# Kernel optimization log

Hardware: AMD Instinct MI355X
Metric: run time of the kernel (lower is better)

The kernel has to match this reference:

```python
import jax, jax.numpy as jnp
import numpy as np

B, N, D, C, H = 32, 36, 2048, 4, 512  # batch, regions, feat dim, coord dim, fusion hidden


def setup_inputs() -> dict:
    key = jax.random.key(0)
    ks = jax.random.split(key, 8)
    w = lambda k, sh: jax.random.normal(k, sh, dtype=jnp.float32) * 0.02
    return {
        "mm": jax.random.normal(ks[0], (B, N, D), dtype=jnp.float32),
        "coords": jax.random.uniform(ks[1], (B, N, C), dtype=jnp.float32),
        # MLB fusion params for coords: z = (x@W_cl * y@W_cr) @ W_cout
        "W_cl": w(ks[2], (C, H)),
        "W_cr": w(ks[3], (C, H)),
        "W_cout": w(ks[4], (H, D)),
        # MLB fusion params for features
        "W_fl": w(ks[5], (D, H)),
        "W_fr": w(ks[6], (D, H)),
        "W_fout": w(ks[7], (H, D)),
    }


def reference(mm, coords, W_cl, W_cr, W_cout, W_fl, W_fr, W_fout):
    # Project once per region (avoids projecting inside the N*N expand).
    cl = coords @ W_cl            # [B,N,H]
    cr = coords @ W_cr            # [B,N,H]
    fl = mm @ W_fl                # [B,N,H]
    fr = mm @ W_fr                # [B,N,H]
    # All-pairs bilinear fusion: Rij = f_coord(c_i, c_j) + f_feat(m_i, m_j)
    pair_c = cl[:, :, None, :] * cr[:, None, :, :]   # [B,N,N,H]
    pair_f = fl[:, :, None, :] * fr[:, None, :, :]   # [B,N,N,H]
    Rij = (jnp.einsum('bijh,hd->bijd', pair_c, W_cout)
           + jnp.einsum('bijh,hd->bijd', pair_f, W_fout))  # [B,N,N,D]
    # agg['type'] == 'max': reduce over the right (j) region axis
    mm_new = Rij.max(axis=2)      # [B,N,D]
    # residual
    return mm_new + mm
```

## Files before the change

### kernel.cpp

```cpp
#include <hip/hip_runtime.h>


typedef __attribute__((ext_vector_type(8))) short short8;
typedef __attribute__((ext_vector_type(4))) short short4v;
typedef __attribute__((ext_vector_type(4))) float f32x4;

__device__ __forceinline__ float bf2f(unsigned short h) {
  return __uint_as_float(((unsigned int)h) << 16);
}
__device__ __forceinline__ unsigned short f2bf(float f) {
  unsigned int u = __float_as_uint(f);
  u += 0x7FFFu + ((u >> 16) & 1u);
  return (unsigned short)(u >> 16);
}
__device__ __forceinline__ void gl2lds16(const void* g, void* l) {
  __builtin_amdgcn_global_load_lds(
      (const __attribute__((address_space(1))) unsigned int*)g,
      (__attribute__((address_space(3))) unsigned int*)l, 16, 0, 0);
}

__global__ __launch_bounds__(256) void k_prep(
    const float* __restrict__ mm, const float* __restrict__ Wfout,
    const float* __restrict__ Wcl, const float* __restrict__ Wcr,
    const float* __restrict__ Wcout, const float* __restrict__ Wfl,
    const float* __restrict__ Wfr, unsigned short* __restrict__ mmb,
    unsigned short* __restrict__ WS, unsigned short* __restrict__ WS2) {
  const int bid = blockIdx.x;
  if (bid < 2304) {
    int idx = bid * 256 + threadIdx.x;
    int row = idx >> 9, h = idx & 511;
    float4 m4 = *(const float4*)(mm + (size_t)row * 2048 + h * 4);
    short4v o;
    o[0] = (short)f2bf(m4.x); o[1] = (short)f2bf(m4.y);
    o[2] = (short)f2bf(m4.z); o[3] = (short)f2bf(m4.w);
    *(short4v*)(mmb + (size_t)row * 2048 + h * 4) = o;
  } else {
    int gi = (bid - 2304) * 256 + threadIdx.x;
    if (gi < 139264) {
      int n = gi & 15, qv = (gi >> 4) & 3, rest = gi >> 6;
      int kc = rest % 17, g2 = rest / 17;
      int d = g2 * 16 + n;
      short8 o;
      if (kc < 16) {
        int kbase = kc * 32 + qv * 8;
        const float* src = Wfout + (size_t)kbase * 2048 + d;
#pragma unroll
        for (int e = 0; e < 8; ++e) o[e] = (short)f2bf(src[(size_t)e * 2048]);
      } else if (qv < 2) {
        float acc[8];
#pragma unroll
        for (int e = 0; e < 8; ++e) acc[e] = 0.f;
        for (int h = 0; h < 512; ++h) {
          float wo = Wcout[(size_t)h * 2048 + d];
          float c0 = Wcl[(qv * 2 + 0) * 512 + h] * wo;
          float c1 = Wcl[(qv * 2 + 1) * 512 + h] * wo;
          float r0 = Wcr[h], r1 = Wcr[512 + h];
          float r2 = Wcr[1024 + h], r3 = Wcr[1536 + h];
          acc[0] += c0 * r0; acc[1] += c0 * r1;
          acc[2] += c0 * r2; acc[3] += c0 * r3;
          acc[4] += c1 * r0; acc[5] += c1 * r1;
          acc[6] += c1 * r2; acc[7] += c1 * r3;
        }
#pragma unroll
        for (int e = 0; e < 8; ++e) o[e] = (short)f2bf(acc[e]);
      } else {
#pragma unroll
        for (int e = 0; e < 8; ++e) o[e] = 0;
      }
      *(short8*)(WS + (size_t)gi * 8) = o;
    } else {
      int gj = gi - 139264;
      int n = gj & 15, qv = (gj >> 4) & 3, kc = (gj >> 6) & 63, cg = gj >> 12;
      int col = cg * 16 + n;
      int dbase = kc * 32 + qv * 8;
      const float* src = (col < 512) ? (Wfl + (size_t)dbase * 512 + col)
                                     : (Wfr + (size_t)dbase * 512 + (col - 512));
      short8 o;
#pragma unroll
      for (int e = 0; e < 8; ++e) o[e] = (short)f2bf(src[(size_t)e * 512]);
      *(short8*)(WS2 + (size_t)gj * 8) = o;
    }
  }
}

__global__ __launch_bounds__(256) void k_proj_feat(
    const unsigned short* __restrict__ mmb, const unsigned short* __restrict__ WS2,
    unsigned short* __restrict__ Fl, unsigned short* __restrict__ Fr) {
  const int tid = threadIdx.x;
  const int lane = tid & 63, w = tid >> 6;
  const int n = lane & 15, q = lane >> 4;
  const int m0 = blockIdx.y * 16;
  const int cg = blockIdx.x * 4 + w;
  const int c0 = cg * 16;

  f32x4 acc = {0.f, 0.f, 0.f, 0.f};
#pragma unroll 4
  for (int kc = 0; kc < 64; ++kc) {
    short8 a = *(const short8*)(mmb + (size_t)(m0 + n) * 2048 + kc * 32 + q * 8);
    short8 b = *(const short8*)(WS2 + (size_t)(cg * 64 + kc) * 512 + lane * 8);
    acc = __builtin_amdgcn_mfma_f32_16x16x32_bf16(a, b, acc, 0, 0, 0);
  }
#pragma unroll
  for (int e = 0; e < 4; ++e) {
    int row = m0 + q * 4 + e;
    int col = c0 + n;
    unsigned short v = f2bf(acc[e]);
    if (col < 512) Fl[(size_t)row * 512 + col] = v;
    else           Fr[(size_t)row * 512 + (col - 512)] = v;
  }
}

__global__ __launch_bounds__(256) void k_prod(
    const unsigned short* __restrict__ Fl, const unsigned short* __restrict__ Fr,
    const float* __restrict__ coords, unsigned short* __restrict__ Pf) {
  int idx = blockIdx.x * 256 + threadIdx.x;
  int lane = idx & 63;
  int gran = idx >> 6;
  int qg = gran / 153;
  int rem = gran - qg * 153;
  int kc = rem / 9;
  int t = rem - kc * 9;
  int n = lane & 15, q = lane >> 4;
  int b = qg / 9;
  int g, j;
  if (t < 8) { g = qg * 4 + (t >> 1); j = (t & 1) * 16 + n; }
  else       { g = qg * 4 + (n >> 2); j = 32 + (n & 3); }
  int rowj = b * 36 + j;
  short8 p;
  if (kc < 16) {
    int k0 = kc * 32 + q * 8;
    short8 cl8 = *(const short8*)(Fl + (size_t)g * 512 + k0);
    short8 cr8 = *(const short8*)(Fr + (size_t)rowj * 512 + k0);
#pragma unroll
    for (int e = 0; e < 8; ++e)
      p[e] = (short)f2bf(bf2f((unsigned short)cl8[e]) * bf2f((unsigned short)cr8[e]));
  } else if (q < 2) {
    float4 ci = *(const float4*)(coords + (size_t)g * 4);
    float4 cj = *(const float4*)(coords + (size_t)rowj * 4);
#pragma unroll
    for (int e = 0; e < 8; ++e) {
      int a = q * 2 + (e >> 2);
      float ca = (a == 0) ? ci.x : (a == 1) ? ci.y : (a == 2) ? ci.z : ci.w;
      float cb = ((e & 3) == 0) ? cj.x : ((e & 3) == 1) ? cj.y
               : ((e & 3) == 2) ? cj.z : cj.w;
      p[e] = (short)f2bf(ca * cb);
    }
  } else {
#pragma unroll
    for (int e = 0; e < 8; ++e) p[e] = 0;
  }
  *(short8*)(Pf + (size_t)idx * 8) = p;
}

__global__ __launch_bounds__(512, 4) void k_pairwise(
    const unsigned short* __restrict__ Pf, const unsigned short* __restrict__ WS,
    const float* __restrict__ mm, float* __restrict__ out) {
  __shared__ __align__(16) unsigned short lB[2][9 * 512];

  const int tid = threadIdx.x;
  const int lane = tid & 63, w = tid >> 6;
  const int n = lane & 15, q = lane >> 4;
  const int bx = blockIdx.x;
  const int x = bx & 7;
  const int m = bx >> 3;
  const int dt = m & 7;
  const int qg = x * 36 + (m >> 3);
  const int g0 = qg * 4;

  f32x4 acc[9][2];
#pragma unroll
  for (int t = 0; t < 9; ++t)
#pragma unroll
    for (int r = 0; r < 2; ++r) acc[t][r] = (f32x4){0.f, 0.f, 0.f, 0.f};

  const unsigned short* Abase = WS + ((size_t)(dt * 16 + w * 2) * 17) * 512 + lane * 8;
  const unsigned short* Bbase = Pf + (size_t)qg * 17 * 9 * 512;

  gl2lds16(Bbase + (size_t)w * 512 + lane * 8, &lB[0][w * 512]);
  if (w == 0) gl2lds16(Bbase + (size_t)8 * 512 + lane * 8, &lB[0][8 * 512]);
  __syncthreads();

#pragma unroll 2
  for (int kc = 0; kc < 16; ++kc) {
    const int buf = kc & 1;
    const unsigned short* bn = Bbase + (size_t)((kc + 1) * 9) * 512 + lane * 8;
    gl2lds16(bn + (size_t)w * 512, &lB[buf ^ 1][w * 512]);
    if (w == 0) gl2lds16(bn + (size_t)8 * 512, &lB[buf ^ 1][8 * 512]);

    short8 a0 = *(const short8*)(Abase + (size_t)kc * 512);
    short8 a1 = *(const short8*)(Abase + (size_t)(17 + kc) * 512);

    short8 bb[9];
#pragma unroll
    for (int t = 0; t < 9; ++t)
      bb[t] = *(const short8*)(&lB[buf][t * 512 + lane * 8]);
#pragma unroll
    for (int t = 0; t < 9; ++t) {
      acc[t][0] = __builtin_amdgcn_mfma_f32_16x16x32_bf16(a0, bb[t], acc[t][0], 0, 0, 0);
      acc[t][1] = __builtin_amdgcn_mfma_f32_16x16x32_bf16(a1, bb[t], acc[t][1], 0, 0, 0);
    }
    __syncthreads();
  }

  {
    short8 a0 = *(const short8*)(Abase + (size_t)16 * 512);
    short8 a1 = *(const short8*)(Abase + (size_t)(17 + 16) * 512);
    short8 bb[9];
#pragma unroll
    for (int t = 0; t < 9; ++t)
      bb[t] = *(const short8*)(&lB[0][t * 512 + lane * 8]);
#pragma unroll
    for (int t = 0; t < 9; ++t) {
      acc[t][0] = __builtin_amdgcn_mfma_f32_16x16x32_bf16(a0, bb[t], acc[t][0], 0, 0, 0);
      acc[t][1] = __builtin_amdgcn_mfma_f32_16x16x32_bf16(a1, bb[t], acc[t][1], 0, 0, 0);
    }
  }

#pragma unroll
  for (int r = 0; r < 2; ++r) {
#pragma unroll
    for (int e = 0; e < 4; ++e) {
      float vs = acc[8][r][e];
#pragma unroll
      for (int ii = 0; ii < 4; ++ii) {
        float v = fmaxf(acc[ii * 2][r][e], acc[ii * 2 + 1][r][e]);
        v = fmaxf(v, ((n >> 2) == ii) ? vs : -1e30f);
#pragma unroll
        for (int s = 1; s < 16; s <<= 1) v = fmaxf(v, __shfl_xor(v, s, 64));
        if (n == 0) {
          int d = dt * 256 + w * 32 + r * 16 + q * 4 + e;
          size_t o = (size_t)(g0 + ii) * 2048 + d;
          out[o] = v + mm[o];
        }
      }
    }
  }
}

extern "C" void kernel_launch(void* const* d_in, const int* in_sizes, int n_in,
                              void* d_out, int out_size, void* d_ws, size_t ws_size,
                              hipStream_t stream) {
  const float* mm     = (const float*)d_in[0];
  const float* coords = (const float*)d_in[1];
  const float* Wcl    = (const float*)d_in[2];
  const float* Wcr    = (const float*)d_in[3];
  const float* Wcout  = (const float*)d_in[4];
  const float* Wfl    = (const float*)d_in[5];
  const float* Wfr    = (const float*)d_in[6];
  const float* Wfout  = (const float*)d_in[7];
  float* out = (float*)d_out;

  unsigned short* Fl  = (unsigned short*)d_ws;
  unsigned short* Fr  = Fl + (size_t)1152 * 512;
  unsigned short* WS  = Fr + (size_t)1152 * 512;
  unsigned short* WS2 = WS + (size_t)139264 * 8;
  unsigned short* mmb = WS2 + (size_t)262144 * 8;
  unsigned short* Pf  = mmb + (size_t)1152 * 2048;

  k_prep<<<2304 + 1568, 256, 0, stream>>>(mm, Wfout, Wcl, Wcr, Wcout,
                                          Wfl, Wfr, mmb, WS, WS2);
  k_proj_feat<<<dim3(16, 72), 256, 0, stream>>>(mmb, WS2, Fl, Fr);
  k_prod<<<11016, 256, 0, stream>>>(Fl, Fr, coords, Pf);
  k_pairwise<<<2304, 512, 0, stream>>>(Pf, WS, mm, out);
}
```

Before: 355.0 us.

## Triple-buffer B tiles, preload ninth tile group, prefetch A fragments one step ahead

Replaces the double-buffered LDS staging with a three-slot ring for the first eight B tiles, so loads run two k-steps ahead. The ninth tile column for all k-steps is loaded into LDS once up front. The A fragments are register-prefetched one step ahead, and the full __syncthreads is swapped for an explicit vmcnt wait plus s_barrier. The goal is to hide global-to-LDS latency and remove stalls at the barrier, at the cost of more LDS per block, which may reduce occupancy.

New measurement: 303.8 us. 14.4% less time.

```diff
diff --git a/kernel.cpp b/kernel.cpp
--- a/kernel.cpp
+++ b/kernel.cpp
@@ -155,7 +155,8 @@
 __global__ __launch_bounds__(512, 4) void k_pairwise(
     const unsigned short* __restrict__ Pf, const unsigned short* __restrict__ WS,
     const float* __restrict__ mm, float* __restrict__ out) {
-  __shared__ __align__(16) unsigned short lB[2][9 * 512];
+  __shared__ __align__(16) unsigned short ring[3][8 * 512];
+  __shared__ __align__(16) unsigned short g8[17 * 512];
 
   const int tid = threadIdx.x;
   const int lane = tid & 63, w = tid >> 6;
@@ -176,45 +177,60 @@
   const unsigned short* Abase = WS + ((size_t)(dt * 16 + w * 2) * 17) * 512 + lane * 8;
   const unsigned short* Bbase = Pf + (size_t)qg * 17 * 9 * 512;
 
-  gl2lds16(Bbase + (size_t)w * 512 + lane * 8, &lB[0][w * 512]);
-  if (w == 0) gl2lds16(Bbase + (size_t)8 * 512 + lane * 8, &lB[0][8 * 512]);
+  short8 a00, a01, a10, a11, a20, a21;
+
+  gl2lds16(Bbase + (size_t)w * 512 + lane * 8, &ring[0][w * 512]);
+  gl2lds16(Bbase + (size_t)(9 + w) * 512 + lane * 8, &ring[1][w * 512]);
+  for (int s = w; s < 17; s += 8)
+    gl2lds16(Bbase + (size_t)(s * 9 + 8) * 512 + lane * 8, &g8[s * 512]);
+  a00 = *(const short8*)(Abase);
+  a01 = *(const short8*)(Abase + 17 * 512);
   __syncthreads();
 
-#pragma unroll 2
-  for (int kc = 0; kc < 16; ++kc) {
-    const int buf = kc & 1;
-    const unsigned short* bn = Bbase + (size_t)((kc + 1) * 9) * 512 + lane * 8;
-    gl2lds16(bn + (size_t)w * 512, &lB[buf ^ 1][w * 512]);
-    if (w == 0) gl2lds16(bn + (size_t)8 * 512, &lB[buf ^ 1][8 * 512]);
-
-    short8 a0 = *(const short8*)(Abase + (size_t)kc * 512);
-    short8 a1 = *(const short8*)(Abase + (size_t)(17 + kc) * 512);
-
-    short8 bb[9];
-#pragma unroll
-    for (int t = 0; t < 9; ++t)
-      bb[t] = *(const short8*)(&lB[buf][t * 512 + lane * 8]);
-#pragma unroll
-    for (int t = 0; t < 9; ++t) {
-      acc[t][0] = __builtin_amdgcn_mfma_f32_16x16x32_bf16(a0, bb[t], acc[t][0], 0, 0, 0);
-      acc[t][1] = __builtin_amdgcn_mfma_f32_16x16x32_bf16(a1, bb[t], acc[t][1], 0, 0, 0);
-    }
-    __syncthreads();
-  }
-
+#define KBODY(C, RU, RS, aU0, aU1, aN0, aN1, DOSTAGE, VMN)                   \
+  {                                                                          \
+    aN0 = *(const short8*)(Abase + (size_t)((C) + 1) * 512);                 \
+    aN1 = *(const short8*)(Abase + (size_t)(17 + (C) + 1) * 512);            \
+    if (DOSTAGE) {                                                           \
+      const unsigned short* bn =                                             \
+          Bbase + (size_t)(((C) + 2) * 9) * 512 + lane * 8;                  \
+      gl2lds16(bn + (size_t)w * 512, &ring[RS][w * 512]);                    \
+    }                                                                        \
+    _Pragma("unroll")                                                        \
+    for (int t = 0; t < 8; ++t) {                                            \
+      short8 bt = *(const short8*)(&ring[RU][t * 512 + lane * 8]);           \
+      acc[t][0] = __builtin_amdgcn_mfma_f32_16x16x32_bf16(aU0, bt, acc[t][0], 0, 0, 0); \
+      acc[t][1] = __builtin_amdgcn_mfma_f32_16x16x32_bf16(aU1, bt, acc[t][1], 0, 0, 0); \
+    }                                                                        \
+    {                                                                        \
+      short8 b8 = *(const short8*)(&g8[(C) * 512 + lane * 8]);               \
+      acc[8][0] = __builtin_amdgcn_mfma_f32_16x16x32_bf16(aU0, b8, acc[8][0], 0, 0, 0); \
+      acc[8][1] = __builtin_amdgcn_mfma_f32_16x16x32_bf16(aU1, b8, acc[8][1], 0, 0, 0); \
+    }                                                                        \
+    asm volatile("s_waitcnt vmcnt(" #VMN ")" ::: "memory");                  \
+    __builtin_amdgcn_s_barrier();                                            \
+  }
+
+  for (int k3 = 0; k3 < 15; k3 += 3) {
+    KBODY(k3 + 0, 0, 2, a00, a01, a10, a11, 1, 3);
+    KBODY(k3 + 1, 1, 0, a10, a11, a20, a21, 1, 3);
+    KBODY(k3 + 2, 2, 1, a20, a21, a00, a01, 1, 3);
+  }
+  KBODY(15, 0, 2, a00, a01, a10, a11, 0, 2);
   {
-    short8 a0 = *(const short8*)(Abase + (size_t)16 * 512);
-    short8 a1 = *(const short8*)(Abase + (size_t)(17 + 16) * 512);
-    short8 bb[9];
-#pragma unroll
-    for (int t = 0; t < 9; ++t)
-      bb[t] = *(const short8*)(&lB[0][t * 512 + lane * 8]);
-#pragma unroll
-    for (int t = 0; t < 9; ++t) {
-      acc[t][0] = __builtin_amdgcn_mfma_f32_16x16x32_bf16(a0, bb[t], acc[t][0], 0, 0, 0);
-      acc[t][1] = __builtin_amdgcn_mfma_f32_16x16x32_bf16(a1, bb[t], acc[t][1], 0, 0, 0);
-    }
-  }
+#pragma unroll
+    for (int t = 0; t < 8; ++t) {
+      short8 bt = *(const short8*)(&ring[1][t * 512 + lane * 8]);
+      acc[t][0] = __builtin_amdgcn_mfma_f32_16x16x32_bf16(a10, bt, acc[t][0], 0, 0, 0);
+      acc[t][1] = __builtin_amdgcn_mfma_f32_16x16x32_bf16(a11, bt, acc[t][1], 0, 0, 0);
+    }
+    {
+      short8 b8 = *(const short8*)(&g8[16 * 512 + lane * 8]);
+      acc[8][0] = __builtin_amdgcn_mfma_f32_16x16x32_bf16(a10, b8, acc[8][0], 0, 0, 0);
+      acc[8][1] = __builtin_amdgcn_mfma_f32_16x16x32_bf16(a11, b8, acc[8][1], 0, 0, 0);
+    }
+  }
+#undef KBODY
 
 #pragma unroll
   for (int r = 0; r < 2; ++r) {
```
